# Performance work log

Measured on AMD Instinct MI355X. Metric: run time of the kernel, lower is better.

The kernel has to match this reference:

```python
import jax, jax.numpy as jnp
import numpy as np

GS = 7        # grid_size
NB = 2        # num_boxes
NC = 20       # num_classes
THR = 0.5     # NMS threshold (source default)
IMG = 448.0   # max_size used in _encode_outputs


def _nms_keep(boxes, scores, valid, thr):
    """Faithful port of the source's (inverted) greedy NMS.

    Picks the highest-score alive box, keeps it, then RETAINS only boxes
    with IoU >= thr against it (discarding low-overlap ones), repeating.
    Fixed-shape: returns a bool keep-mask of length N.
    """
    N = scores.shape[0]
    x1, y1, x2, y2 = boxes[:, 0], boxes[:, 1], boxes[:, 2], boxes[:, 3]
    areas = (x2 - x1) * (y2 - y1)
    neg = jnp.asarray(-1e30, scores.dtype)
    idx = jnp.arange(N)

    def step(carry, _):
        alive, keep = carry
        any_alive = jnp.any(alive)
        i = jnp.argmax(jnp.where(alive, scores, neg))
        keep = keep | ((idx == i) & any_alive)
        ix1 = jnp.maximum(x1, x1[i]); iy1 = jnp.maximum(y1, y1[i])
        ix2 = jnp.minimum(x2, x2[i]); iy2 = jnp.minimum(y2, y2[i])
        inter = jnp.clip(ix2 - ix1, 0) * jnp.clip(iy2 - iy1, 0)
        iou = inter / (areas[i] + areas - inter)
        new_alive = (alive & (iou >= thr)) & (idx != i)
        alive = jnp.where(any_alive, new_alive, alive)
        return (alive, keep), None

    (_, keep), _ = jax.lax.scan(step, (valid, jnp.zeros(N, bool)), None, length=N)
    return keep


def _forward(x, W, b):
    B = x.shape[0]
    out = (x @ W.T + b).reshape(B, GS, GS, 5 * NB + NC)  # (B,7,7,30)
    cell = 1.0 / GS
    g = jnp.arange(GS, dtype=out.dtype) * cell
    norm_x = g[None, None, :]   # varies along last grid axis (grid_x[r,c]=c)
    norm_y = g[None, :, None]

    labels = out[..., 5 * NB:]                                # (B,7,7,20)
    labels_proba = jnp.argmax(labels, -1).astype(out.dtype)   # class index

    N = B * GS * GS
    labels_flat = labels.reshape(N, NC)

    slot_boxes, slot_scores, slot_valid = [], [], []
    for off in range(0, 5 * NB, 5):
        bx = out[..., off:off + 4]
        sc = out[..., off + 5]                 # faithful off-by-one in source
        valid = (sc * labels_proba) > 0.5      # faithful score*class_index mask
        cx = bx[..., 0] * cell + norm_x
        cy = bx[..., 1] * cell + norm_y
        w_, h_ = bx[..., 2], bx[..., 3]
        X1 = cx - 0.5 * w_; Y1 = cy - 0.5 * h_
        X2 = cx + 0.5 * w_; Y2 = cy + 0.5 * h_
        # NMS applies xywh2xyxy AGAIN on already-xyxy boxes (faithful):
        bb = jnp.stack([X1 - X2 / 2, Y1 - Y2 / 2, X1 + X2 / 2, Y1 + Y2 / 2], -1)
        slot_boxes.append(bb.reshape(N, 4))
        slot_scores.append(sc.reshape(N))
        slot_valid.append(valid.reshape(N))

    boxes = jnp.stack(slot_boxes)     # (NB, N, 4)
    scores = jnp.stack(slot_scores)   # (NB, N)
    valid = jnp.stack(slot_valid)     # (NB, N)

    keep = jax.vmap(_nms_keep, in_axes=(0, 0, 0, None))(boxes, scores, valid, THR)

    labels_all = jnp.broadcast_to(labels_flat[None], (NB, N, NC))
    packed = jnp.concatenate([boxes * IMG, scores[..., None], labels_all], -1)
    return packed * keep[..., None].astype(packed.dtype)  # (NB, N, 25)


def setup_inputs() -> dict:
    key = jax.random.key(0)
    k1, k2, k3 = jax.random.split(key, 3)
    B = 64
    x = jax.random.normal(k1, (B, 2304), jnp.float32)
    W = jax.random.normal(k2, (1470, 2304), jnp.float32) * 0.02
    b = jax.random.normal(k3, (1470,), jnp.float32) * 0.01
    return {"x": x, "W": W, "b": b}


def reference(x, W, b):
    return _forward(x, W, b)
```

## Files before the change

### kernel.cpp

```cpp
#include <hip/hip_runtime.h>

#define B_     64
#define KDIM   2304
#define NCOL   1470
#define NCELL  3136
#define CPAD   1536
#define SPLITK 16
#define KCHUNK 144
#define NSTAGE 9

__global__ __launch_bounds__(256) void gemm_splitk(
    const float* __restrict__ x, const float* __restrict__ W,
    float* __restrict__ partial)
{
    __shared__ float sx[16 * 68];
    __shared__ float sw[16 * 100];

    const int t   = threadIdx.x;
    const int c0  = blockIdx.x * 96;
    const int k0  = blockIdx.y * KCHUNK;
    const int r8  = (t >> 5) << 3;
    const int cgi = t & 31;
    const int kk0 = t & 15;
    const int g0  = t >> 4;

    float acc[8][3];
#pragma unroll
    for (int i = 0; i < 8; ++i)
#pragma unroll
        for (int j = 0; j < 3; ++j) acc[i][j] = 0.f;

    float xr[4], wr[6];
    {
        const int kb = k0;
#pragma unroll
        for (int p = 0; p < 4; ++p)
            xr[p] = x[(p * 16 + g0) * KDIM + kb + kk0];
#pragma unroll
        for (int p = 0; p < 6; ++p) {
            int gc = c0 + p * 16 + g0;
            if (gc >= NCOL) gc = NCOL - 1;
            wr[p] = W[(size_t)gc * KDIM + kb + kk0];
        }
    }

    for (int s = 0; s < NSTAGE; ++s) {
        __syncthreads();
#pragma unroll
        for (int p = 0; p < 4; ++p) sx[kk0 * 68 + p * 16 + g0] = xr[p];
#pragma unroll
        for (int p = 0; p < 6; ++p) sw[kk0 * 100 + p * 16 + g0] = wr[p];
        __syncthreads();
        if (s + 1 < NSTAGE) {
            const int kb = k0 + ((s + 1) << 4);
#pragma unroll
            for (int p = 0; p < 4; ++p)
                xr[p] = x[(p * 16 + g0) * KDIM + kb + kk0];
#pragma unroll
            for (int p = 0; p < 6; ++p) {
                int gc = c0 + p * 16 + g0;
                if (gc >= NCOL) gc = NCOL - 1;
                wr[p] = W[(size_t)gc * KDIM + kb + kk0];
            }
        }
#pragma unroll
        for (int kk = 0; kk < 16; ++kk) {
            const float4 a0 = *(const float4*)&sx[kk * 68 + r8];
            const float4 a1 = *(const float4*)&sx[kk * 68 + r8 + 4];
            const float w0 = sw[kk * 100 + cgi];
            const float w1 = sw[kk * 100 + cgi + 32];
            const float w2 = sw[kk * 100 + cgi + 64];
            const float av[8] = {a0.x, a0.y, a0.z, a0.w, a1.x, a1.y, a1.z, a1.w};
#pragma unroll
            for (int i = 0; i < 8; ++i) {
                acc[i][0] = fmaf(av[i], w0, acc[i][0]);
                acc[i][1] = fmaf(av[i], w1, acc[i][1]);
                acc[i][2] = fmaf(av[i], w2, acc[i][2]);
            }
        }
    }

    float* pb = partial + (size_t)blockIdx.y * (B_ * CPAD) + c0 + cgi;
#pragma unroll
    for (int i = 0; i < 8; ++i)
#pragma unroll
        for (int p = 0; p < 3; ++p)
            pb[(size_t)(r8 + i) * CPAD + 32 * p] = acc[i][p];
}

__global__ __launch_bounds__(256) void combine_prep(
    const float* __restrict__ partial, const float* __restrict__ bias,
    float* __restrict__ labels, float* __restrict__ boxes,
    float* __restrict__ scores, int* __restrict__ valid)
{
    __shared__ float sa[8][30];
    const int t    = threadIdx.x;
    const int base = blockIdx.x * 8;

    if (t < 240) {
        const int n   = base + t / 30;
        const int col = t % 30;
        const int row = n / 49;
        const int cr  = (n % 49) * 30 + col;
        float s = 0.f;
#pragma unroll
        for (int k = 0; k < SPLITK; ++k)
            s += partial[(size_t)k * (B_ * CPAD) + (size_t)row * CPAD + cr];
        s += bias[cr];
        sa[t / 30][col] = s;
        if (col >= 10) labels[(size_t)n * 20 + (col - 10)] = s;
    }
    __syncthreads();

    if (t < 8) {
        const int n = base + t;
        const float* a = sa[t];
        float mv = a[10]; int mi = 0;
#pragma unroll
        for (int j = 1; j < 20; ++j) {
            float v = a[10 + j];
            if (v > mv) { mv = v; mi = j; }
        }
        const float lp = (float)mi;
        const int gx = n % 7, gy = (n / 7) % 7;
        const float cw = 1.0f / 7.0f;
        const float nx = (float)gx * cw, ny = (float)gy * cw;
#pragma unroll
        for (int sl = 0; sl < 2; ++sl) {
            const int off = 5 * sl;
            const float bx0 = a[off], bx1 = a[off + 1];
            const float w_ = a[off + 2], h_ = a[off + 3];
            const float sc = a[off + 5];
            const float cx = bx0 * cw + nx, cy = bx1 * cw + ny;
            const float X1 = cx - 0.5f * w_, Y1 = cy - 0.5f * h_;
            const float X2 = cx + 0.5f * w_, Y2 = cy + 0.5f * h_;
            const int m = sl * NCELL + n;
            boxes[m * 4 + 0] = X1 - 0.5f * X2;
            boxes[m * 4 + 1] = Y1 - 0.5f * Y2;
            boxes[m * 4 + 2] = X1 + 0.5f * X2;
            boxes[m * 4 + 3] = Y1 + 0.5f * Y2;
            scores[m] = sc;
            valid[m] = (sc * lp > 0.5f) ? 1 : 0;
        }
    }
}

__global__ __launch_bounds__(1024) void nms_kernel(
    const float* __restrict__ boxes, const float* __restrict__ scores,
    const int* __restrict__ valid, float* __restrict__ keep)
{
    __shared__ float bx1[NCELL], by1[NCELL], bx2[NCELL], by2[NCELL];
    __shared__ float ssc[NCELL];
    __shared__ int   lstA[NCELL], lstB[NCELL];
    __shared__ unsigned char kp[NCELL];
    __shared__ float rv[16];
    __shared__ int   ri[16];
    __shared__ int   cA, cB, spick;

    const int slot = blockIdx.x;
    const int base = slot * NCELL;
    const int t = threadIdx.x;

    if (t == 0) { cA = 0; cB = 0; }
    __syncthreads();
    for (int n = t; n < NCELL; n += 1024) {
        const float4 bb = *(const float4*)&boxes[(size_t)(base + n) * 4];
        bx1[n] = bb.x; by1[n] = bb.y; bx2[n] = bb.z; by2[n] = bb.w;
        ssc[n] = scores[base + n];
        kp[n] = 0;
        if (valid[base + n]) { int p = atomicAdd(&cA, 1); lstA[p] = n; }
    }
    __syncthreads();

    int* cur = lstA; int* nxt = lstB;
    int curIsA = 1;
    for (;;) {
        const int cnt = curIsA ? cA : cB;

        float bv = -1e30f; int bi = 0x7fffffff;
        for (int j = t; j < cnt; j += 1024) {
            const int n = cur[j];
            const float v = ssc[n];
            if (v > bv || (v == bv && n < bi)) { bv = v; bi = n; }
        }
#pragma unroll
        for (int o = 32; o > 0; o >>= 1) {
            const float ov = __shfl_down(bv, o);
            const int   oi = __shfl_down(bi, o);
            if (ov > bv || (ov == bv && oi < bi)) { bv = ov; bi = oi; }
        }
        if ((t & 63) == 0) { rv[t >> 6] = bv; ri[t >> 6] = bi; }
        __syncthreads();
        if (t == 0) {
            float v2 = rv[0]; int i2 = ri[0];
#pragma unroll
            for (int q = 1; q < 16; ++q)
                if (rv[q] > v2 || (rv[q] == v2 && ri[q] < i2)) { v2 = rv[q]; i2 = ri[q]; }
            spick = (v2 == -1e30f) ? -1 : i2;
            if (curIsA) cB = 0; else cA = 0;
        }
        __syncthreads();
        const int i = spick;
        if (i < 0) break;
        if (t == 0) kp[i] = 1;

        const float xi1 = bx1[i], yi1 = by1[i], xi2 = bx2[i], yi2 = by2[i];
        const float ai  = (xi2 - xi1) * (yi2 - yi1);

        int* nxtCnt = curIsA ? &cB : &cA;
        for (int j = t; j < cnt; j += 1024) {
            const int n = cur[j];
            const float x1 = bx1[n], y1 = by1[n], x2 = bx2[n], y2 = by2[n];
            const float an = (x2 - x1) * (y2 - y1);
            const float ix1 = fmaxf(x1, xi1), iy1 = fmaxf(y1, yi1);
            const float ix2 = fminf(x2, xi2), iy2 = fminf(y2, yi2);
            const float inter = fmaxf(ix2 - ix1, 0.f) * fmaxf(iy2 - iy1, 0.f);
            const float iou = inter / (ai + an - inter);
            if (iou >= 0.5f && n != i) { int p = atomicAdd(nxtCnt, 1); nxt[p] = n; }
        }
        __syncthreads();
        { int* tmp = cur; cur = nxt; nxt = tmp; }
        curIsA ^= 1;
    }

    for (int n = t; n < NCELL; n += 1024)
        keep[base + n] = (float)kp[n];
}

__global__ void pack_out(const float* __restrict__ labels,
                         const float* __restrict__ boxes,
                         const float* __restrict__ scores,
                         const float* __restrict__ keep,
                         float* __restrict__ out)
{
    int idx = blockIdx.x * 256 + threadIdx.x;
    if (idx >= 2 * NCELL * 25) return;
    int c  = idx % 25;
    int sn = idx / 25;
    int n  = sn % NCELL;
    float k = keep[sn];
    float v;
    if (c < 4)       v = boxes[(size_t)sn * 4 + c] * 448.0f;
    else if (c == 4) v = scores[sn];
    else             v = labels[(size_t)n * 20 + (c - 5)];
    out[idx] = v * k;
}

extern "C" void kernel_launch(void* const* d_in, const int* in_sizes, int n_in,
                              void* d_out, int out_size, void* d_ws, size_t ws_size,
                              hipStream_t stream)
{
    const float* x = (const float*)d_in[0];
    const float* W = (const float*)d_in[1];
    const float* b = (const float*)d_in[2];
    float* out = (float*)d_out;

    float* ws      = (float*)d_ws;
    float* partial = ws;
    float* labels  = partial + (size_t)SPLITK * B_ * CPAD;
    float* boxes   = labels + (size_t)NCELL * 20;
    float* scores  = boxes + (size_t)NCELL * 8;
    int*   valid   = (int*)(scores + (size_t)NCELL * 2);
    float* keep    = (float*)(valid + (size_t)NCELL * 2);

    hipLaunchKernelGGL(gemm_splitk, dim3(16, SPLITK), dim3(256), 0, stream,
                       x, W, partial);
    hipLaunchKernelGGL(combine_prep, dim3(NCELL / 8), dim3(256), 0, stream,
                       partial, b, labels, boxes, scores, valid);
    hipLaunchKernelGGL(nms_kernel, dim3(2), dim3(1024), 0, stream,
                       boxes, scores, valid, keep);
    hipLaunchKernelGGL(pack_out, dim3((2 * NCELL * 25 + 255) / 256), dim3(256), 0, stream,
                       labels, boxes, scores, keep, out);
}
```

Measured before the change: 34.12 us.

## Double-buffer GEMM shared tiles and fuse output packing into NMS kernel

The split-K GEMM now uses two shared-memory buffers so the next tile is stored while the current one is consumed, removing one barrier per stage. The separate pack_out kernel is folded into the NMS kernel, which writes the final packed output directly from shared-memory boxes and scores and the keep flags. This removes a launch and the intermediate keep buffer. The risk is that packing 2×3136×25 outputs from only two blocks may be slower than the wide grid used before.

```diff
diff --git a/kernel.cpp b/kernel.cpp
--- a/kernel.cpp
+++ b/kernel.cpp
@@ -8,13 +8,15 @@
 #define SPLITK 16
 #define KCHUNK 144
 #define NSTAGE 9
+#define XS     68
+#define WS     100
 
 __global__ __launch_bounds__(256) void gemm_splitk(
     const float* __restrict__ x, const float* __restrict__ W,
     float* __restrict__ partial)
 {
-    __shared__ float sx[16 * 68];
-    __shared__ float sw[16 * 100];
+    __shared__ float sx[2][16 * XS];
+    __shared__ float sw[2][16 * WS];
 
     const int t   = threadIdx.x;
     const int c0  = blockIdx.x * 96;
@@ -30,46 +32,47 @@
 #pragma unroll
         for (int j = 0; j < 3; ++j) acc[i][j] = 0.f;
 
+    const float* wp[6];
+#pragma unroll
+    for (int p = 0; p < 6; ++p) {
+        int gc = c0 + p * 16 + g0;
+        if (gc >= NCOL) gc = NCOL - 1;
+        wp[p] = W + (size_t)gc * KDIM + kk0;
+    }
+    const float* xp = x + (size_t)g0 * 16 * 0 + kk0;
+
     float xr[4], wr[6];
     {
         const int kb = k0;
 #pragma unroll
-        for (int p = 0; p < 4; ++p)
-            xr[p] = x[(p * 16 + g0) * KDIM + kb + kk0];
-#pragma unroll
-        for (int p = 0; p < 6; ++p) {
-            int gc = c0 + p * 16 + g0;
-            if (gc >= NCOL) gc = NCOL - 1;
-            wr[p] = W[(size_t)gc * KDIM + kb + kk0];
-        }
+        for (int p = 0; p < 4; ++p) xr[p] = x[(p * 16 + g0) * KDIM + kb + kk0];
+#pragma unroll
+        for (int p = 0; p < 6; ++p) wr[p] = wp[p][kb];
+#pragma unroll
+        for (int p = 0; p < 4; ++p) sx[0][kk0 * XS + p * 16 + g0] = xr[p];
+#pragma unroll
+        for (int p = 0; p < 6; ++p) sw[0][kk0 * WS + p * 16 + g0] = wr[p];
     }
 
     for (int s = 0; s < NSTAGE; ++s) {
-        __syncthreads();
-#pragma unroll
-        for (int p = 0; p < 4; ++p) sx[kk0 * 68 + p * 16 + g0] = xr[p];
-#pragma unroll
-        for (int p = 0; p < 6; ++p) sw[kk0 * 100 + p * 16 + g0] = wr[p];
-        __syncthreads();
+        const int cb = s & 1;
         if (s + 1 < NSTAGE) {
             const int kb = k0 + ((s + 1) << 4);
 #pragma unroll
-            for (int p = 0; p < 4; ++p)
-                xr[p] = x[(p * 16 + g0) * KDIM + kb + kk0];
-#pragma unroll
-            for (int p = 0; p < 6; ++p) {
-                int gc = c0 + p * 16 + g0;
-                if (gc >= NCOL) gc = NCOL - 1;
-                wr[p] = W[(size_t)gc * KDIM + kb + kk0];
-            }
-        }
+            for (int p = 0; p < 4; ++p) xr[p] = x[(p * 16 + g0) * KDIM + kb + kk0];
+#pragma unroll
+            for (int p = 0; p < 6; ++p) wr[p] = wp[p][kb];
+        }
+        __syncthreads();
+        const float* cx = sx[cb];
+        const float* cw = sw[cb];
 #pragma unroll
         for (int kk = 0; kk < 16; ++kk) {
-            const float4 a0 = *(const float4*)&sx[kk * 68 + r8];
-            const float4 a1 = *(const float4*)&sx[kk * 68 + r8 + 4];
-            const float w0 = sw[kk * 100 + cgi];
-            const float w1 = sw[kk * 100 + cgi + 32];
-            const float w2 = sw[kk * 100 + cgi + 64];
+            const float4 a0 = *(const float4*)&cx[kk * XS + r8];
+            const float4 a1 = *(const float4*)&cx[kk * XS + r8 + 4];
+            const float w0 = cw[kk * WS + cgi];
+            const float w1 = cw[kk * WS + cgi + 32];
+            const float w2 = cw[kk * WS + cgi + 64];
             const float av[8] = {a0.x, a0.y, a0.z, a0.w, a1.x, a1.y, a1.z, a1.w};
 #pragma unroll
             for (int i = 0; i < 8; ++i) {
@@ -77,6 +80,12 @@
                 acc[i][1] = fmaf(av[i], w1, acc[i][1]);
                 acc[i][2] = fmaf(av[i], w2, acc[i][2]);
             }
+        }
+        if (s + 1 < NSTAGE) {
+#pragma unroll
+            for (int p = 0; p < 4; ++p) sx[cb ^ 1][kk0 * XS + p * 16 + g0] = xr[p];
+#pragma unroll
+            for (int p = 0; p < 6; ++p) sw[cb ^ 1][kk0 * WS + p * 16 + g0] = wr[p];
         }
     }
 
@@ -145,9 +154,10 @@
     }
 }
 
-__global__ __launch_bounds__(1024) void nms_kernel(
+__global__ __launch_bounds__(1024) void nms_pack(
     const float* __restrict__ boxes, const float* __restrict__ scores,
-    const int* __restrict__ valid, float* __restrict__ keep)
+    const int* __restrict__ valid, const float* __restrict__ labels,
+    float* __restrict__ out)
 {
     __shared__ float bx1[NCELL], by1[NCELL], bx2[NCELL], by2[NCELL];
     __shared__ float ssc[NCELL];
@@ -223,27 +233,21 @@
         curIsA ^= 1;
     }
 
-    for (int n = t; n < NCELL; n += 1024)
-        keep[base + n] = (float)kp[n];
-}
-
-__global__ void pack_out(const float* __restrict__ labels,
-                         const float* __restrict__ boxes,
-                         const float* __restrict__ scores,
-                         const float* __restrict__ keep,
-                         float* __restrict__ out)
-{
-    int idx = blockIdx.x * 256 + threadIdx.x;
-    if (idx >= 2 * NCELL * 25) return;
-    int c  = idx % 25;
-    int sn = idx / 25;
-    int n  = sn % NCELL;
-    float k = keep[sn];
-    float v;
-    if (c < 4)       v = boxes[(size_t)sn * 4 + c] * 448.0f;
-    else if (c == 4) v = scores[sn];
-    else             v = labels[(size_t)n * 20 + (c - 5)];
-    out[idx] = v * k;
+    float* os = out + (size_t)base * 25;
+    for (int li = t; li < NCELL * 25; li += 1024) {
+        const int n = li / 25;
+        const int c = li % 25;
+        const float k = (float)kp[n];
+        float v;
+        if (c < 4) {
+            v = (c == 0 ? bx1[n] : c == 1 ? by1[n] : c == 2 ? bx2[n] : by2[n]) * 448.0f;
+        } else if (c == 4) {
+            v = ssc[n];
+        } else {
+            v = labels[(size_t)n * 20 + (c - 5)];
+        }
+        os[li] = v * k;
+    }
 }
 
 extern "C" void kernel_launch(void* const* d_in, const int* in_sizes, int n_in,
@@ -261,14 +265,11 @@
     float* boxes   = labels + (size_t)NCELL * 20;
     float* scores  = boxes + (size_t)NCELL * 8;
     int*   valid   = (int*)(scores + (size_t)NCELL * 2);
-    float* keep    = (float*)(valid + (size_t)NCELL * 2);
 
     hipLaunchKernelGGL(gemm_splitk, dim3(16, SPLITK), dim3(256), 0, stream,
                        x, W, partial);
     hipLaunchKernelGGL(combine_prep, dim3(NCELL / 8), dim3(256), 0, stream,
                        partial, b, labels, boxes, scores, valid);
-    hipLaunchKernelGGL(nms_kernel, dim3(2), dim3(1024), 0, stream,
-                       boxes, scores, valid, keep);
-    hipLaunchKernelGGL(pack_out, dim3((2 * NCELL * 25 + 255) / 256), dim3(256), 0, stream,
-                       labels, boxes, scores, keep, out);
-}
+    hipLaunchKernelGGL(nms_pack, dim3(2), dim3(1024), 0, stream,
+                       boxes, scores, valid, labels, out);
+}
```

Result: slower. 70.12 us (+105.5%).

## Double-buffer GEMM shared tiles and keep NMS alive set in register bitmasks

Applied to the files above, without the earlier changes.

The split-K GEMM now uses two shared-memory buffers, so the next tile is written to the alternate buffer after compute. This cuts the per-stage syncthreads from two to one. The NMS kernel drops its atomic-compacted index lists and instead holds each thread's alive boxes as a per-thread bitmask over a fixed stride of cells. This removes the shared atomics and list-swap bookkeeping, but every iteration now scans a fixed four slots per thread whether or not they are alive. Double buffering also doubles GEMM shared memory.

```diff
diff --git a/kernel.cpp b/kernel.cpp
--- a/kernel.cpp
+++ b/kernel.cpp
@@ -8,13 +8,17 @@
 #define SPLITK 16
 #define KCHUNK 144
 #define NSTAGE 9
+#define XS     68
+#define WSD    100
+#define NMS_T  1024
+#define QMAX   4
 
 __global__ __launch_bounds__(256) void gemm_splitk(
     const float* __restrict__ x, const float* __restrict__ W,
     float* __restrict__ partial)
 {
-    __shared__ float sx[16 * 68];
-    __shared__ float sw[16 * 100];
+    __shared__ float sx[2][16 * XS];
+    __shared__ float sw[2][16 * WSD];
 
     const int t   = threadIdx.x;
     const int c0  = blockIdx.x * 96;
@@ -30,46 +34,46 @@
 #pragma unroll
         for (int j = 0; j < 3; ++j) acc[i][j] = 0.f;
 
+    const float* wp[6];
+#pragma unroll
+    for (int p = 0; p < 6; ++p) {
+        int gc = c0 + p * 16 + g0;
+        if (gc >= NCOL) gc = NCOL - 1;
+        wp[p] = W + (size_t)gc * KDIM + kk0;
+    }
+
     float xr[4], wr[6];
     {
         const int kb = k0;
 #pragma unroll
-        for (int p = 0; p < 4; ++p)
-            xr[p] = x[(p * 16 + g0) * KDIM + kb + kk0];
-#pragma unroll
-        for (int p = 0; p < 6; ++p) {
-            int gc = c0 + p * 16 + g0;
-            if (gc >= NCOL) gc = NCOL - 1;
-            wr[p] = W[(size_t)gc * KDIM + kb + kk0];
-        }
+        for (int p = 0; p < 4; ++p) xr[p] = x[(p * 16 + g0) * KDIM + kb + kk0];
+#pragma unroll
+        for (int p = 0; p < 6; ++p) wr[p] = wp[p][kb];
+#pragma unroll
+        for (int p = 0; p < 4; ++p) sx[0][kk0 * XS + p * 16 + g0] = xr[p];
+#pragma unroll
+        for (int p = 0; p < 6; ++p) sw[0][kk0 * WSD + p * 16 + g0] = wr[p];
     }
 
     for (int s = 0; s < NSTAGE; ++s) {
-        __syncthreads();
-#pragma unroll
-        for (int p = 0; p < 4; ++p) sx[kk0 * 68 + p * 16 + g0] = xr[p];
-#pragma unroll
-        for (int p = 0; p < 6; ++p) sw[kk0 * 100 + p * 16 + g0] = wr[p];
-        __syncthreads();
+        const int cb = s & 1;
         if (s + 1 < NSTAGE) {
             const int kb = k0 + ((s + 1) << 4);
 #pragma unroll
-            for (int p = 0; p < 4; ++p)
-                xr[p] = x[(p * 16 + g0) * KDIM + kb + kk0];
-#pragma unroll
-            for (int p = 0; p < 6; ++p) {
-                int gc = c0 + p * 16 + g0;
-                if (gc >= NCOL) gc = NCOL - 1;
-                wr[p] = W[(size_t)gc * KDIM + kb + kk0];
-            }
-        }
+            for (int p = 0; p < 4; ++p) xr[p] = x[(p * 16 + g0) * KDIM + kb + kk0];
+#pragma unroll
+            for (int p = 0; p < 6; ++p) wr[p] = wp[p][kb];
+        }
+        __syncthreads();
+        const float* cx = sx[cb];
+        const float* cw = sw[cb];
 #pragma unroll
         for (int kk = 0; kk < 16; ++kk) {
-            const float4 a0 = *(const float4*)&sx[kk * 68 + r8];
-            const float4 a1 = *(const float4*)&sx[kk * 68 + r8 + 4];
-            const float w0 = sw[kk * 100 + cgi];
-            const float w1 = sw[kk * 100 + cgi + 32];
-            const float w2 = sw[kk * 100 + cgi + 64];
+            const float4 a0 = *(const float4*)&cx[kk * XS + r8];
+            const float4 a1 = *(const float4*)&cx[kk * XS + r8 + 4];
+            const float w0 = cw[kk * WSD + cgi];
+            const float w1 = cw[kk * WSD + cgi + 32];
+            const float w2 = cw[kk * WSD + cgi + 64];
             const float av[8] = {a0.x, a0.y, a0.z, a0.w, a1.x, a1.y, a1.z, a1.w};
 #pragma unroll
             for (int i = 0; i < 8; ++i) {
@@ -77,6 +81,12 @@
                 acc[i][1] = fmaf(av[i], w1, acc[i][1]);
                 acc[i][2] = fmaf(av[i], w2, acc[i][2]);
             }
+        }
+        if (s + 1 < NSTAGE) {
+#pragma unroll
+            for (int p = 0; p < 4; ++p) sx[cb ^ 1][kk0 * XS + p * 16 + g0] = xr[p];
+#pragma unroll
+            for (int p = 0; p < 6; ++p) sw[cb ^ 1][kk0 * WSD + p * 16 + g0] = wr[p];
         }
     }
 
@@ -145,85 +155,81 @@
     }
 }
 
-__global__ __launch_bounds__(1024) void nms_kernel(
+__global__ __launch_bounds__(NMS_T) void nms_kernel(
     const float* __restrict__ boxes, const float* __restrict__ scores,
     const int* __restrict__ valid, float* __restrict__ keep)
 {
-    __shared__ float bx1[NCELL], by1[NCELL], bx2[NCELL], by2[NCELL];
-    __shared__ float ssc[NCELL];
-    __shared__ int   lstA[NCELL], lstB[NCELL];
+    __shared__ float sX1[NCELL], sY1[NCELL], sX2[NCELL], sY2[NCELL];
+    __shared__ float sSc[NCELL];
     __shared__ unsigned char kp[NCELL];
     __shared__ float rv[16];
-    __shared__ int   ri[16];
-    __shared__ int   cA, cB, spick;
+    __shared__ int   rn[16];
+    __shared__ int   pickN;
 
     const int slot = blockIdx.x;
     const int base = slot * NCELL;
     const int t = threadIdx.x;
 
-    if (t == 0) { cA = 0; cB = 0; }
+    unsigned am = 0;
+#pragma unroll
+    for (int q = 0; q < QMAX; ++q) {
+        const int n = t + q * NMS_T;
+        if (n < NCELL) {
+            const float4 bb = *(const float4*)&boxes[(size_t)(base + n) * 4];
+            sX1[n] = bb.x; sY1[n] = bb.y; sX2[n] = bb.z; sY2[n] = bb.w;
+            sSc[n] = scores[base + n];
+            kp[n] = 0;
+            if (valid[base + n]) am |= 1u << q;
+        }
+    }
     __syncthreads();
-    for (int n = t; n < NCELL; n += 1024) {
-        const float4 bb = *(const float4*)&boxes[(size_t)(base + n) * 4];
-        bx1[n] = bb.x; by1[n] = bb.y; bx2[n] = bb.z; by2[n] = bb.w;
-        ssc[n] = scores[base + n];
-        kp[n] = 0;
-        if (valid[base + n]) { int p = atomicAdd(&cA, 1); lstA[p] = n; }
-    }
-    __syncthreads();
-
-    int* cur = lstA; int* nxt = lstB;
-    int curIsA = 1;
+
     for (;;) {
-        const int cnt = curIsA ? cA : cB;
-
-        float bv = -1e30f; int bi = 0x7fffffff;
-        for (int j = t; j < cnt; j += 1024) {
-            const int n = cur[j];
-            const float v = ssc[n];
-            if (v > bv || (v == bv && n < bi)) { bv = v; bi = n; }
-        }
+        float bv = -1e30f; int bn = 0x7fffffff;
+#pragma unroll
+        for (int q = 0; q < QMAX; ++q)
+            if ((am >> q) & 1u) {
+                const int n = t + q * NMS_T;
+                const float v = sSc[n];
+                if (v > bv || (v == bv && n < bn)) { bv = v; bn = n; }
+            }
 #pragma unroll
         for (int o = 32; o > 0; o >>= 1) {
             const float ov = __shfl_down(bv, o);
-            const int   oi = __shfl_down(bi, o);
-            if (ov > bv || (ov == bv && oi < bi)) { bv = ov; bi = oi; }
-        }
-        if ((t & 63) == 0) { rv[t >> 6] = bv; ri[t >> 6] = bi; }
+            const int   on = __shfl_down(bn, o);
+            if (ov > bv || (ov == bv && on < bn)) { bv = ov; bn = on; }
+        }
+        if ((t & 63) == 0) { rv[t >> 6] = bv; rn[t >> 6] = bn; }
         __syncthreads();
         if (t == 0) {
-            float v2 = rv[0]; int i2 = ri[0];
+            float v2 = rv[0]; int n2 = rn[0];
 #pragma unroll
             for (int q = 1; q < 16; ++q)
-                if (rv[q] > v2 || (rv[q] == v2 && ri[q] < i2)) { v2 = rv[q]; i2 = ri[q]; }
-            spick = (v2 == -1e30f) ? -1 : i2;
-            if (curIsA) cB = 0; else cA = 0;
+                if (rv[q] > v2 || (rv[q] == v2 && rn[q] < n2)) { v2 = rv[q]; n2 = rn[q]; }
+            if (v2 == -1e30f) { pickN = -1; }
+            else { pickN = n2; kp[n2] = 1; }
         }
         __syncthreads();
-        const int i = spick;
-        if (i < 0) break;
-        if (t == 0) kp[i] = 1;
-
-        const float xi1 = bx1[i], yi1 = by1[i], xi2 = bx2[i], yi2 = by2[i];
-        const float ai  = (xi2 - xi1) * (yi2 - yi1);
-
-        int* nxtCnt = curIsA ? &cB : &cA;
-        for (int j = t; j < cnt; j += 1024) {
-            const int n = cur[j];
-            const float x1 = bx1[n], y1 = by1[n], x2 = bx2[n], y2 = by2[n];
-            const float an = (x2 - x1) * (y2 - y1);
-            const float ix1 = fmaxf(x1, xi1), iy1 = fmaxf(y1, yi1);
-            const float ix2 = fminf(x2, xi2), iy2 = fminf(y2, yi2);
-            const float inter = fmaxf(ix2 - ix1, 0.f) * fmaxf(iy2 - iy1, 0.f);
-            const float iou = inter / (ai + an - inter);
-            if (iou >= 0.5f && n != i) { int p = atomicAdd(nxtCnt, 1); nxt[p] = n; }
-        }
-        __syncthreads();
-        { int* tmp = cur; cur = nxt; nxt = tmp; }
-        curIsA ^= 1;
-    }
-
-    for (int n = t; n < NCELL; n += 1024)
+        const int pn = pickN;
+        if (pn < 0) break;
+        const float px1 = sX1[pn], py1 = sY1[pn], px2 = sX2[pn], py2 = sY2[pn];
+        const float pa = (px2 - px1) * (py2 - py1);
+
+#pragma unroll
+        for (int q = 0; q < QMAX; ++q)
+            if ((am >> q) & 1u) {
+                const int n = t + q * NMS_T;
+                const float x1 = sX1[n], y1 = sY1[n], x2 = sX2[n], y2 = sY2[n];
+                const float an = (x2 - x1) * (y2 - y1);
+                const float ix1 = fmaxf(x1, px1), iy1 = fmaxf(y1, py1);
+                const float ix2 = fminf(x2, px2), iy2 = fminf(y2, py2);
+                const float inter = fmaxf(ix2 - ix1, 0.f) * fmaxf(iy2 - iy1, 0.f);
+                const float iou = inter / (pa + an - inter);
+                if (!(iou >= 0.5f) || n == pn) am &= ~(1u << q);
+            }
+    }
+
+    for (int n = t; n < NCELL; n += NMS_T)
         keep[base + n] = (float)kp[n];
 }
 
@@ -267,7 +273,7 @@
                        x, W, partial);
     hipLaunchKernelGGL(combine_prep, dim3(NCELL / 8), dim3(256), 0, stream,
                        partial, b, labels, boxes, scores, valid);
-    hipLaunchKernelGGL(nms_kernel, dim3(2), dim3(1024), 0, stream,
+    hipLaunchKernelGGL(nms_kernel, dim3(2), dim3(NMS_T), 0, stream,
                        boxes, scores, valid, keep);
     hipLaunchKernelGGL(pack_out, dim3((2 * NCELL * 25 + 255) / 256), dim3(256), 0, stream,
                        labels, boxes, scores, keep, out);
```

After: 33.04 us. 1.03x faster.
